# Kernel tuning notes

Measured on AMD Instinct MI355X. Metric: run time of the kernel, lower is better.

## Reference

```python
import jax, jax.numpy as jnp
import numpy as np

SIZES = [11793, 2948, 737, 184]   # vertices per mesh level, fine -> coarse
SPIRAL = [20, 14, 12, 9]          # spiral length per level
FILT = [128, 128, 64, 3]          # filters_dec[0]
LATENT = 128
BATCH = 16


def setup_inputs() -> dict:
    key = jax.random.key(0)
    ks = jax.random.split(key, 12)
    V = [s + 1 for s in SIZES]  # +1 dummy vertex per level
    inp = {}
    inp["z"] = jax.random.normal(ks[0], (BATCH, LATENT), jnp.float32)
    # dense upsampling matrices: level k+1 -> level k
    inp["U0"] = jax.random.normal(ks[1], (V[0], V[1]), jnp.float32) * 0.02
    inp["U1"] = jax.random.normal(ks[2], (V[1], V[2]), jnp.float32) * 0.02
    inp["U2"] = jax.random.normal(ks[3], (V[2], V[3]), jnp.float32) * 0.02
    # spiral index tables per level (shared across batch, values in [0, V))
    inp["S0"] = jax.random.randint(ks[4], (V[0], SPIRAL[0]), 0, V[0], dtype=jnp.int32)
    inp["S1"] = jax.random.randint(ks[5], (V[1], SPIRAL[1]), 0, V[1], dtype=jnp.int32)
    inp["S2"] = jax.random.randint(ks[6], (V[2], SPIRAL[2]), 0, V[2], dtype=jnp.int32)
    # fc_latent_dec: latent -> (sizes[-1]+1)*filters_dec[0][0]
    inp["Wfc"] = jax.random.normal(ks[7], (LATENT, V[3] * FILT[0]), jnp.float32) * 0.02
    inp["bfc"] = jnp.zeros((V[3] * FILT[0],), jnp.float32)
    # SpiralConv linear weights, stored (K*F_in, F_out), K-major flatten as in torch
    inp["W0"] = jax.random.normal(ks[8], (SPIRAL[2] * FILT[0], FILT[1]), jnp.float32) * 0.02
    inp["b0"] = jnp.zeros((FILT[1],), jnp.float32)
    inp["W1"] = jax.random.normal(ks[9], (SPIRAL[1] * FILT[1], FILT[2]), jnp.float32) * 0.02
    inp["b1"] = jnp.zeros((FILT[2],), jnp.float32)
    inp["W2"] = jax.random.normal(ks[10], (SPIRAL[0] * FILT[2], FILT[3]), jnp.float32) * 0.02
    inp["b2"] = jnp.zeros((FILT[3],), jnp.float32)
    return inp


def spiral_conv(x, S, W, b, elu):
    # x: (B, V, F); S: (V, K) vertex indices into the same level
    B, V, F = x.shape
    K = S.shape[1]
    g = jnp.take(x, S.reshape(-1), axis=1).reshape(B, V, K * F)  # gather, K-major flatten
    out = g @ W + b  # (B, V, F_out)
    if elu:
        out = jax.nn.elu(out)
    # zero out the dummy (last) vertex, as in Neural3DMM's zero_padding mask
    return out.at[:, -1, :].set(0.0)


def reference(z, U0, U1, U2, S0, S1, S2, Wfc, bfc, W0, b0, W1, b1, W2, b2):
    B = z.shape[0]
    x = (z @ Wfc + bfc).reshape(B, SIZES[-1] + 1, FILT[0])  # (B, 185, 128)
    x = jnp.einsum('vw,bwf->bvf', U2, x)                    # upsample -> (B, 738, 128)
    x = spiral_conv(x, S2, W0, b0, True)                    # (B, 738, 128)
    x = jnp.einsum('vw,bwf->bvf', U1, x)                    # (B, 2949, 128)
    x = spiral_conv(x, S1, W1, b1, True)                    # (B, 2949, 64)
    x = jnp.einsum('vw,bwf->bvf', U0, x)                    # (B, 11794, 64)
    x = spiral_conv(x, S0, W2, b2, False)                   # identity act -> (B, 11794, 3)
    return x
```

## Files before the change

kernel.cpp:

```cpp
#include <hip/hip_runtime.h>
#include <cmath>


#define NB 16

typedef __attribute__((ext_vector_type(8))) short bf16x8;
typedef __attribute__((ext_vector_type(4))) float f32x4;

__device__ __forceinline__ unsigned short f2bf(float x) {
    union { float f; unsigned u; } v; v.f = x;
    unsigned r = v.u + 0x7FFFu + ((v.u >> 16) & 1u);
    return (unsigned short)(r >> 16);
}
__device__ __forceinline__ void gload16(const void* src, void* dst) {
    __builtin_amdgcn_global_load_lds(
        (const __attribute__((address_space(1))) unsigned int*)src,
        (__attribute__((address_space(3))) unsigned int*)dst, 16, 0, 0);
}

__global__ __launch_bounds__(256) void cvt_u_all(
    const float* __restrict__ U0, const float* __restrict__ U1,
    const float* __restrict__ U2, unsigned short* __restrict__ Ub0,
    unsigned short* __restrict__ Ub1, unsigned short* __restrict__ Ub2) {
    int k = blockIdx.x * 256 + threadIdx.x;
    int r = blockIdx.y;
    const float* src;
    unsigned short* dst;
    int V, W, Wp, row;
    if (r < 11904) {
        src = U0; dst = Ub0; V = 11794; W = 2949; Wp = 2976; row = r;
    } else if (r < 11904 + 3072) {
        src = U1; dst = Ub1; V = 2949; W = 738; Wp = 768; row = r - 11904;
    } else {
        src = U2; dst = Ub2; V = 738; W = 185; Wp = 192; row = r - 11904 - 3072;
    }
    if (k >= Wp) return;
    float v = (row < V && k < W) ? src[(size_t)row * W + k] : 0.f;
    dst[(size_t)row * Wp + k] = f2bf(v);
}

__global__ __launch_bounds__(256) void cvt_misc(
    const float* __restrict__ W0, const float* __restrict__ W1,
    const float* __restrict__ W2, const int* __restrict__ S0,
    const int* __restrict__ S1, const int* __restrict__ S2,
    unsigned short* __restrict__ W0T, unsigned short* __restrict__ W1T,
    unsigned short* __restrict__ W2T, int* __restrict__ S0T,
    int* __restrict__ S1T, int* __restrict__ S2T) {
    const int N0 = 128 * 1536, N1 = 64 * 1792, N2 = 16 * 1288;
    const int N3 = 20 * 11794, N4 = 14 * 2949, N5 = 12 * 738;
    int id = blockIdx.x * 256 + threadIdx.x;
    if (id < N0) {
        int n = id / 1536, k = id - n * 1536;
        W0T[id] = f2bf(W0[(size_t)k * 128 + n]);
        return;
    }
    id -= N0;
    if (id < N1) {
        int n = id / 1792, k = id - n * 1792;
        W1T[id] = f2bf(W1[(size_t)k * 64 + n]);
        return;
    }
    id -= N1;
    if (id < N2) {
        int n = id / 1288, k = id - n * 1288;
        float v = (n < 3 && k < 1280) ? W2[(size_t)k * 3 + n] : 0.f;
        W2T[id] = f2bf(v);
        return;
    }
    id -= N2;
    if (id < N3) {
        int k = id / 11794, v = id - k * 11794;
        S0T[id] = S0[(size_t)v * 20 + k];
        return;
    }
    id -= N3;
    if (id < N4) {
        int k = id / 2949, v = id - k * 2949;
        S1T[id] = S1[(size_t)v * 14 + k];
        return;
    }
    id -= N4;
    if (id < N5) {
        int k = id / 738, v = id - k * 738;
        S2T[id] = S2[(size_t)v * 12 + k];
    }
}

__global__ __launch_bounds__(256) void fc_kernel(const float* __restrict__ z,
                                                 const float* __restrict__ Wfc,
                                                 const float* __restrict__ bfc,
                                                 unsigned short* __restrict__ x3T) {
    const int N = 185 * 128;
    __shared__ float zs[NB * 128];
    int t = threadIdx.x;
    for (int i = t; i < NB * 128; i += 256) zs[i] = z[i];
    __syncthreads();
    int n = blockIdx.x * 256 + t;
    if (n >= N) return;
    float acc[NB];
#pragma unroll
    for (int b = 0; b < NB; ++b) acc[b] = 0.f;
    for (int k = 0; k < 128; ++k) {
        float w = Wfc[k * N + n];
#pragma unroll
        for (int b = 0; b < NB; ++b) acc[b] = fmaf(zs[b * 128 + k], w, acc[b]);
    }
    float bv = bfc[n];
    int f = n & 127, v = n >> 7;
#pragma unroll
    for (int b = 0; b < NB; ++b)
        x3T[(size_t)(b * 128 + f) * 192 + v] = f2bf(acc[b] + bv);
    if (n < 7 * 128) {
        int vp = 185 + (n >> 7);
#pragma unroll
        for (int b = 0; b < NB; ++b)
            x3T[(size_t)(b * 128 + f) * 192 + vp] = 0;
    }
}

template<int FSH, int VP>
__global__ __launch_bounds__(256) void ups_mfma(
    const unsigned short* __restrict__ Ub, const unsigned short* __restrict__ xT,
    unsigned short* __restrict__ out,
    int WpA, int WpB, int nsteps, int gxsh, int q) {
    const int F = 1 << FSH;
    __shared__ __align__(16) unsigned short As[3][128 * 32];
    __shared__ __align__(16) unsigned short Bs[3][128 * 32];
    const int t = threadIdx.x;
    const int wv = t >> 6, lane = t & 63;
    const int lr = lane & 15;

    const int flat = blockIdx.x;
    const int wg = (flat & 7) * q + (flat >> 3);
    const int m0 = (wg >> gxsh) * 128;
    const int n0 = (wg & ((1 << gxsh) - 1)) * 128;

    const int srow = lane >> 2;
    const int schunk = (((lane & 3) - ((lane >> 3) & 3)) & 3) * 8;
    const int ii0 = wv * 2, ii1 = wv * 2 + 1;
    const unsigned short* asrc0 = Ub + (size_t)(m0 + ii0 * 16 + srow) * WpA + schunk;
    const unsigned short* asrc1 = Ub + (size_t)(m0 + ii1 * 16 + srow) * WpA + schunk;
    const unsigned short* bsrc0 = xT + (size_t)(n0 + ii0 * 16 + srow) * WpB + schunk;
    const unsigned short* bsrc1 = xT + (size_t)(n0 + ii1 * 16 + srow) * WpB + schunk;

    const int fslot = (((lane >> 4) + (lr >> 1)) & 3) * 8;
    const int wrow = (wv >> 1) * 64;
    const int wcol = (wv & 1) * 64;
    const int u0 = wv * 1024;

    f32x4 acc[4][4];
#pragma unroll
    for (int i = 0; i < 4; ++i)
#pragma unroll
        for (int j = 0; j < 4; ++j) acc[i][j] = {0.f, 0.f, 0.f, 0.f};

#define UPS_STAGE(off_, B_)                                             \
    {                                                                   \
        gload16(asrc0 + (off_), &As[B_][u0]);                           \
        gload16(bsrc0 + (off_), &Bs[B_][u0]);                           \
        gload16(asrc1 + (off_), &As[B_][u0 + 512]);                     \
        gload16(bsrc1 + (off_), &Bs[B_][u0 + 512]);                     \
    }
#define UPS_COMPUTE(B_)                                                 \
    {                                                                   \
        bf16x8 af[4], bg[4];                                            \
        _Pragma("unroll")                                               \
        for (int mt = 0; mt < 4; ++mt)                                  \
            af[mt] = *(const bf16x8*)&As[B_][(wrow + mt * 16 + lr) * 32 + fslot]; \
        _Pragma("unroll")                                               \
        for (int nt = 0; nt < 4; ++nt)                                  \
            bg[nt] = *(const bf16x8*)&Bs[B_][(wcol + nt * 16 + lr) * 32 + fslot]; \
        _Pragma("unroll")                                               \
        for (int mt = 0; mt < 4; ++mt)                                  \
            _Pragma("unroll")                                           \
            for (int nt = 0; nt < 4; ++nt)                              \
                acc[mt][nt] = __builtin_amdgcn_mfma_f32_16x16x32_bf16(  \
                    af[mt], bg[nt], acc[mt][nt], 0, 0, 0);              \
    }
#define UPS_WAIT4 asm volatile("s_waitcnt vmcnt(4)" ::: "memory"); __builtin_amdgcn_s_barrier();
#define UPS_WAIT0 asm volatile("s_waitcnt vmcnt(0)" ::: "memory"); __builtin_amdgcn_s_barrier();

    UPS_STAGE(0, 0);
    UPS_STAGE(32, 1);
    UPS_WAIT4;

    const int m = nsteps / 3;
    for (int it = 0; it < m - 1; ++it) {
        UPS_STAGE(64, 2);  UPS_COMPUTE(0); UPS_WAIT4;
        UPS_STAGE(96, 0);  UPS_COMPUTE(1); UPS_WAIT4;
        UPS_STAGE(128, 1); UPS_COMPUTE(2); UPS_WAIT4;
        asrc0 += 96; asrc1 += 96; bsrc0 += 96; bsrc1 += 96;
    }
    UPS_STAGE(64, 2);
    UPS_COMPUTE(0); UPS_WAIT4;
    UPS_COMPUTE(1); UPS_WAIT0;
    UPS_COMPUTE(2);
#undef UPS_STAGE
#undef UPS_COMPUTE
#undef UPS_WAIT4
#undef UPS_WAIT0

#pragma unroll
    for (int mt = 0; mt < 4; ++mt) {
        const int vb = m0 + wrow + mt * 16 + (lane >> 4) * 4;
#pragma unroll
        for (int nt = 0; nt < 4; ++nt) {
            const int col = n0 + wcol + nt * 16 + lr;
            const int b = col >> FSH, f = col & (F - 1);
            unsigned short* op = out + (size_t)b * VP * F + f;
#pragma unroll
            for (int j = 0; j < 4; ++j)
                op[(size_t)(vb + j) * F] = f2bf(acc[mt][nt][j]);
        }
    }
}

template<int VP, int NSTEPS, int KSP>
__global__ __launch_bounds__(64) void conv_mfma(
    const unsigned short* __restrict__ xu, const int* __restrict__ ST,
    const unsigned short* __restrict__ WT, const float* __restrict__ bias,
    unsigned short* __restrict__ outT,
    int VT, int Kdim, int Fout) {
    __shared__ __align__(16) unsigned short As[2][32 * 32];
    __shared__ __align__(16) unsigned short Bs[3][64 * 32];
    const int lane = threadIdx.x;
    const int lr = lane & 15;
    const int m0 = blockIdx.x * 32;
    const int n0 = blockIdx.y * 64;
    const int b = m0 / VP;
    const int v0 = m0 - b * VP;
    const unsigned short* xb = xu + (((size_t)b * VP) << 7);

    const int arow = lane >> 1;
    const int h = lane & 1;
    const int vg = (v0 + arow < VT) ? (v0 + arow) : (VT - 1);
    const int schunk = (((lane & 3) - ((lane >> 3) & 3)) & 3) * 8;
    const int fslot = (((lane >> 4) + (lr >> 1)) & 3) * 8;
    const int sw0 = arow * 32 + (((2 * h + 0 + ((lane >> 2) & 3)) & 3) * 8);
    const int sw1 = arow * 32 + (((2 * h + 1 + ((lane >> 2) & 3)) & 3) * 8);

    int idx[KSP];
#pragma unroll
    for (int k = 0; k < KSP; ++k) idx[k] = ST[(size_t)k * VT + vg];

    f32x4 acc[2][4];
#pragma unroll
    for (int i = 0; i < 2; ++i)
#pragma unroll
        for (int j = 0; j < 4; ++j) acc[i][j] = {0.f, 0.f, 0.f, 0.f};

    bf16x8 gA[2][2];

#define CC(AB_, BB_)                                                    \
    {                                                                   \
        bf16x8 af[2], bg[4];                                            \
        _Pragma("unroll")                                               \
        for (int mt = 0; mt < 2; ++mt)                                  \
            af[mt] = *(const bf16x8*)&As[AB_][(mt * 16 + lr) * 32 + fslot]; \
        _Pragma("unroll")                                               \
        for (int nt = 0; nt < 4; ++nt)                                  \
            bg[nt] = *(const bf16x8*)&Bs[BB_][(nt * 16 + lr) * 32 + fslot]; \
        _Pragma("unroll")                                               \
        for (int mt = 0; mt < 2; ++mt)                                  \
            _Pragma("unroll")                                           \
            for (int nt = 0; nt < 4; ++nt)                              \
                acc[mt][nt] = __builtin_amdgcn_mfma_f32_16x16x32_bf16(  \
                    af[mt], bg[nt], acc[mt][nt], 0, 0, 0);              \
    }

    {
        const unsigned short* p = xb + (((size_t)idx[0]) << 7) + h * 16;
        gA[0][0] = *(const bf16x8*)(p);
        gA[0][1] = *(const bf16x8*)(p + 8);
#pragma unroll
        for (int i = 0; i < 4; ++i) {
            const int n = n0 + i * 16 + (lane >> 2);
            gload16(WT + (size_t)n * Kdim + schunk, &Bs[0][i * 512]);
        }
#pragma unroll
        for (int i = 0; i < 4; ++i) {
            const int n = n0 + i * 16 + (lane >> 2);
            gload16(WT + (size_t)n * Kdim + 32 + schunk, &Bs[1][i * 512]);
        }
        *(bf16x8*)&As[0][sw0] = gA[0][0];
        *(bf16x8*)&As[0][sw1] = gA[0][1];
        asm volatile("s_waitcnt vmcnt(4)" ::: "memory");
    }

#pragma unroll
    for (int ts = 0; ts < NSTEPS - 2; ++ts) {
        const int tn1 = ts + 1, tn2 = ts + 2;
        {
            const unsigned short* p =
                xb + (((size_t)idx[tn1 >> 2]) << 7) + (tn1 & 3) * 32 + h * 16;
            gA[tn1 & 1][0] = *(const bf16x8*)(p);
            gA[tn1 & 1][1] = *(const bf16x8*)(p + 8);
        }
        {
            const int k0 = tn2 * 32;
#pragma unroll
            for (int i = 0; i < 4; ++i) {
                const int n = n0 + i * 16 + (lane >> 2);
                gload16(WT + (size_t)n * Kdim + k0 + schunk, &Bs[tn2 % 3][i * 512]);
            }
        }
        CC(ts & 1, ts % 3);
        asm volatile("s_waitcnt vmcnt(4)" ::: "memory");
        *(bf16x8*)&As[tn1 & 1][sw0] = gA[tn1 & 1][0];
        *(bf16x8*)&As[tn1 & 1][sw1] = gA[tn1 & 1][1];
    }
    {
        const int tn1 = NSTEPS - 1;
        const unsigned short* p =
            xb + (((size_t)idx[tn1 >> 2]) << 7) + (tn1 & 3) * 32 + h * 16;
        gA[tn1 & 1][0] = *(const bf16x8*)(p);
        gA[tn1 & 1][1] = *(const bf16x8*)(p + 8);
        CC((NSTEPS - 2) & 1, (NSTEPS - 2) % 3);
        asm volatile("s_waitcnt vmcnt(0)" ::: "memory");
        *(bf16x8*)&As[tn1 & 1][sw0] = gA[tn1 & 1][0];
        *(bf16x8*)&As[tn1 & 1][sw1] = gA[tn1 & 1][1];
    }
    CC((NSTEPS - 1) & 1, (NSTEPS - 1) % 3);
#undef CC

#pragma unroll
    for (int nt = 0; nt < 4; ++nt) {
        const int n = n0 + nt * 16 + lr;
        const float bv = bias[n];
        unsigned short* op = outT + (size_t)(b * Fout + n) * VP;
#pragma unroll
        for (int mt = 0; mt < 2; ++mt) {
            const int v = v0 + mt * 16 + (lane >> 4) * 4;
            ushort4 stv;
#pragma unroll
            for (int j = 0; j < 4; ++j) {
                float val = acc[mt][nt][j] + bv;
                val = val > 0.f ? val : expm1f(val);
                if (v + j == VT - 1) val = 0.f;
                ((unsigned short*)&stv)[j] = f2bf(val);
            }
            *(ushort4*)(op + v) = stv;
        }
    }
}

__global__ __launch_bounds__(64) void out_mfma(
    const unsigned short* __restrict__ xu, const int* __restrict__ ST,
    const unsigned short* __restrict__ W2T, const float* __restrict__ b2,
    float* __restrict__ out) {
    const int VT = 11794, VP = 11904, TPB = 372, NSTEPS = 40;
    __shared__ __align__(16) unsigned short As[2][32 * 32];
    const int lane = threadIdx.x;
    const int lr = lane & 15;
    const int lko = (lane >> 4) * 8;
    const int bm = blockIdx.x;
    const int b = bm / TPB;
    const int v0 = (bm - b * TPB) * 32;
    const unsigned short* xb = xu + ((size_t)b * VP << 6);

    const int arow = lane >> 1;
    const int h = lane & 1;
    const int v = v0 + arow;
    const int vg = v < VT ? v : VT - 1;
    const int sw0 = arow * 32 + (((2 * h + 0 + ((lane >> 2) & 3)) & 3) * 8);
    const int sw1 = arow * 32 + (((2 * h + 1 + ((lane >> 2) & 3)) & 3) * 8);
    const int fslot = (((lane >> 4) + (lr >> 1)) & 3) * 8;

    int idx[20];
#pragma unroll
    for (int k = 0; k < 20; ++k) idx[k] = ST[(size_t)k * VT + vg];

    f32x4 acc[2];
    acc[0] = {0.f, 0.f, 0.f, 0.f};
    acc[1] = {0.f, 0.f, 0.f, 0.f};

    const unsigned short* wrow = W2T + (size_t)lr * 1288 + lko;
    bf16x8 gA[2][2], bgr[2];

#define OC(AB_, WB_)                                                    \
    {                                                                   \
        bf16x8 af[2];                                                   \
        _Pragma("unroll")                                               \
        for (int mt = 0; mt < 2; ++mt)                                  \
            af[mt] = *(const bf16x8*)&As[AB_][(mt * 16 + lr) * 32 + fslot]; \
        _Pragma("unroll")                                               \
        for (int mt = 0; mt < 2; ++mt)                                  \
            acc[mt] = __builtin_amdgcn_mfma_f32_16x16x32_bf16(          \
                af[mt], bgr[WB_], acc[mt], 0, 0, 0);                    \
    }

    {
        const unsigned short* p = xb + (((size_t)idx[0]) << 6) + h * 16;
        gA[0][0] = *(const bf16x8*)(p);
        gA[0][1] = *(const bf16x8*)(p + 8);
        bgr[0] = *(const bf16x8*)(wrow);
        *(bf16x8*)&As[0][sw0] = gA[0][0];
        *(bf16x8*)&As[0][sw1] = gA[0][1];
    }

#pragma unroll
    for (int ts = 0; ts < NSTEPS - 1; ++ts) {
        const int tn = ts + 1;
        const unsigned short* p =
            xb + (((size_t)idx[tn >> 1]) << 6) + (tn & 1) * 32 + h * 16;
        gA[tn & 1][0] = *(const bf16x8*)(p);
        gA[tn & 1][1] = *(const bf16x8*)(p + 8);
        bgr[tn & 1] = *(const bf16x8*)(wrow + tn * 32);
        OC(ts & 1, ts & 1);
        *(bf16x8*)&As[tn & 1][sw0] = gA[tn & 1][0];
        *(bf16x8*)&As[tn & 1][sw1] = gA[tn & 1][1];
    }
    OC((NSTEPS - 1) & 1, (NSTEPS - 1) & 1);
#undef OC

    if (lr < 3) {
        const float bv = b2[lr];
#pragma unroll
        for (int mt = 0; mt < 2; ++mt) {
#pragma unroll
            for (int j = 0; j < 4; ++j) {
                const int vv = v0 + mt * 16 + (lane >> 4) * 4 + j;
                if (vv < VT) {
                    float val = acc[mt][j] + bv;
                    if (vv == VT - 1) val = 0.f;
                    out[((size_t)b * VT + vv) * 3 + lr] = val;
                }
            }
        }
    }
}

extern "C" void kernel_launch(void* const* d_in, const int* in_sizes, int n_in,
                              void* d_out, int out_size, void* d_ws, size_t ws_size,
                              hipStream_t stream) {
    const float* z   = (const float*)d_in[0];
    const float* U0  = (const float*)d_in[1];
    const float* U1  = (const float*)d_in[2];
    const float* U2  = (const float*)d_in[3];
    const int*   S0  = (const int*)d_in[4];
    const int*   S1  = (const int*)d_in[5];
    const int*   S2  = (const int*)d_in[6];
    const float* Wfc = (const float*)d_in[7];
    const float* bfc = (const float*)d_in[8];
    const float* W0  = (const float*)d_in[9];
    const float* b0  = (const float*)d_in[10];
    const float* W1  = (const float*)d_in[11];
    const float* b1  = (const float*)d_in[12];
    const float* W2  = (const float*)d_in[13];
    const float* b2  = (const float*)d_in[14];
    float* out = (float*)d_out;

    char* ws = (char*)d_ws;
    unsigned short* Ub0 = (unsigned short*)(ws + 0);
    unsigned short* Ub1 = (unsigned short*)(ws + 70852608);
    unsigned short* Ub2 = (unsigned short*)(ws + 75571200);
    unsigned short* x3T = (unsigned short*)(ws + 75866112);
    unsigned short* x2u = (unsigned short*)(ws + 76652544);
    unsigned short* x2T = (unsigned short*)(ws + 79798272);
    unsigned short* x1u = (unsigned short*)(ws + 82944000);
    unsigned short* x1T = (unsigned short*)(ws + 95526912);
    unsigned short* x0u = (unsigned short*)(ws + 101818368);
    unsigned short* W0T = (unsigned short*)(ws + 126197760);
    unsigned short* W1T = (unsigned short*)(ws + 126590976);
    int* S1T = (int*)(ws + 126820352);
    int* S2T = (int*)(ws + 126985504);
    int* S0T = (int*)(ws + 127020928);
    unsigned short* W2T = (unsigned short*)(ws + 127964448);

    cvt_u_all<<<dim3(12, 11904 + 3072 + 768), 256, 0, stream>>>(U0, U1, U2, Ub0, Ub1, Ub2);
    {
        const int total = 128 * 1536 + 64 * 1792 + 16 * 1288 +
                          20 * 11794 + 14 * 2949 + 12 * 738;
        cvt_misc<<<dim3((total + 255) / 256), 256, 0, stream>>>(
            W0, W1, W2, S0, S1, S2, W0T, W1T, W2T, S0T, S1T, S2T);
    }

    fc_kernel<<<dim3((185 * 128 + 255) / 256), 256, 0, stream>>>(z, Wfc, bfc, x3T);
    ups_mfma<7, 768><<<dim3(96), 256, 0, stream>>>(Ub2, x3T, x2u, 192, 192, 6, 4, 12);
    conv_mfma<768, 48, 12><<<dim3(384, 2), 64, 0, stream>>>(
        x2u, S2T, W0T, b0, x2T, 738, 1536, 128);
    ups_mfma<7, 3072><<<dim3(384), 256, 0, stream>>>(Ub1, x2T, x1u, 768, 768, 24, 4, 48);
    conv_mfma<3072, 56, 14><<<dim3(1536, 1), 64, 0, stream>>>(
        x1u, S1T, W1T, b1, x1T, 2949, 1792, 64);
    ups_mfma<6, 11904><<<dim3(744), 256, 0, stream>>>(Ub0, x1T, x0u, 2976, 3072, 93, 3, 93);
    out_mfma<<<dim3(16 * 372), 64, 0, stream>>>(x0u, S0T, W2T, b2, out);
}
```

Measured before the change: 353.6 us.

## Halve upsample GEMM N-tile and pack U conversion into grid-stride pairs

The upsampling MFMA kernel now uses 128x64 output tiles instead of 128x128, doubling the workgroup count for each level to improve occupancy and CU coverage. The cost is reloading A tiles twice as often. The fp32-to-bf16 conversion of the dense upsampling matrices now runs as a fixed 2048-block grid-stride kernel. Each thread converts two elements and writes one packed 32-bit word, replacing a huge 2D grid with one thread per element.

```diff
diff --git a/kernel.cpp b/kernel.cpp
--- a/kernel.cpp
+++ b/kernel.cpp
@@ -20,23 +20,43 @@
 
 __global__ __launch_bounds__(256) void cvt_u_all(
     const float* __restrict__ U0, const float* __restrict__ U1,
-    const float* __restrict__ U2, unsigned short* __restrict__ Ub0,
-    unsigned short* __restrict__ Ub1, unsigned short* __restrict__ Ub2) {
-    int k = blockIdx.x * 256 + threadIdx.x;
-    int r = blockIdx.y;
-    const float* src;
-    unsigned short* dst;
-    int V, W, Wp, row;
-    if (r < 11904) {
-        src = U0; dst = Ub0; V = 11794; W = 2949; Wp = 2976; row = r;
-    } else if (r < 11904 + 3072) {
-        src = U1; dst = Ub1; V = 2949; W = 738; Wp = 768; row = r - 11904;
-    } else {
-        src = U2; dst = Ub2; V = 738; W = 185; Wp = 192; row = r - 11904 - 3072;
-    }
-    if (k >= Wp) return;
-    float v = (row < V && k < W) ? src[(size_t)row * W + k] : 0.f;
-    dst[(size_t)row * Wp + k] = f2bf(v);
+    const float* __restrict__ U2, unsigned int* __restrict__ Ub0,
+    unsigned int* __restrict__ Ub1, unsigned int* __restrict__ Ub2) {
+    const unsigned nth = gridDim.x * 256u;
+    const unsigned tid = blockIdx.x * 256u + threadIdx.x;
+    for (unsigned p = tid; p < 11904u * 1488u; p += nth) {
+        unsigned row = p / 1488u;
+        unsigned k = (p - row * 1488u) * 2u;
+        float v0 = 0.f, v1 = 0.f;
+        if (row < 11794u) {
+            const float* s = U0 + (size_t)row * 2949u + k;
+            if (k < 2949u) v0 = s[0];
+            if (k + 1u < 2949u) v1 = s[1];
+        }
+        Ub0[p] = (unsigned)f2bf(v0) | ((unsigned)f2bf(v1) << 16);
+    }
+    for (unsigned p = tid; p < 3072u * 384u; p += nth) {
+        unsigned row = p / 384u;
+        unsigned k = (p - row * 384u) * 2u;
+        float v0 = 0.f, v1 = 0.f;
+        if (row < 2949u) {
+            const float* s = U1 + (size_t)row * 738u + k;
+            if (k < 738u) v0 = s[0];
+            if (k + 1u < 738u) v1 = s[1];
+        }
+        Ub1[p] = (unsigned)f2bf(v0) | ((unsigned)f2bf(v1) << 16);
+    }
+    for (unsigned p = tid; p < 768u * 96u; p += nth) {
+        unsigned row = p / 96u;
+        unsigned k = (p - row * 96u) * 2u;
+        float v0 = 0.f, v1 = 0.f;
+        if (row < 738u) {
+            const float* s = U2 + (size_t)row * 185u + k;
+            if (k < 185u) v0 = s[0];
+            if (k + 1u < 185u) v1 = s[1];
+        }
+        Ub2[p] = (unsigned)f2bf(v0) | ((unsigned)f2bf(v1) << 16);
+    }
 }
 
 __global__ __launch_bounds__(256) void cvt_misc(
@@ -125,7 +145,7 @@
     int WpA, int WpB, int nsteps, int gxsh, int q) {
     const int F = 1 << FSH;
     __shared__ __align__(16) unsigned short As[3][128 * 32];
-    __shared__ __align__(16) unsigned short Bs[3][128 * 32];
+    __shared__ __align__(16) unsigned short Bs[3][64 * 32];
     const int t = threadIdx.x;
     const int wv = t >> 6, lane = t & 63;
     const int lr = lane & 15;
@@ -133,78 +153,77 @@
     const int flat = blockIdx.x;
     const int wg = (flat & 7) * q + (flat >> 3);
     const int m0 = (wg >> gxsh) * 128;
-    const int n0 = (wg & ((1 << gxsh) - 1)) * 128;
+    const int n0 = (wg & ((1 << gxsh) - 1)) * 64;
 
     const int srow = lane >> 2;
     const int schunk = (((lane & 3) - ((lane >> 3) & 3)) & 3) * 8;
     const int ii0 = wv * 2, ii1 = wv * 2 + 1;
     const unsigned short* asrc0 = Ub + (size_t)(m0 + ii0 * 16 + srow) * WpA + schunk;
     const unsigned short* asrc1 = Ub + (size_t)(m0 + ii1 * 16 + srow) * WpA + schunk;
-    const unsigned short* bsrc0 = xT + (size_t)(n0 + ii0 * 16 + srow) * WpB + schunk;
-    const unsigned short* bsrc1 = xT + (size_t)(n0 + ii1 * 16 + srow) * WpB + schunk;
+    const unsigned short* bsrc0 = xT + (size_t)(n0 + wv * 16 + srow) * WpB + schunk;
 
     const int fslot = (((lane >> 4) + (lr >> 1)) & 3) * 8;
     const int wrow = (wv >> 1) * 64;
-    const int wcol = (wv & 1) * 64;
+    const int wcol = (wv & 1) * 32;
     const int u0 = wv * 1024;
-
-    f32x4 acc[4][4];
+    const int ub0 = wv * 512;
+
+    f32x4 acc[4][2];
 #pragma unroll
     for (int i = 0; i < 4; ++i)
 #pragma unroll
-        for (int j = 0; j < 4; ++j) acc[i][j] = {0.f, 0.f, 0.f, 0.f};
+        for (int j = 0; j < 2; ++j) acc[i][j] = {0.f, 0.f, 0.f, 0.f};
 
 #define UPS_STAGE(off_, B_)                                             \
     {                                                                   \
         gload16(asrc0 + (off_), &As[B_][u0]);                           \
-        gload16(bsrc0 + (off_), &Bs[B_][u0]);                           \
+        gload16(bsrc0 + (off_), &Bs[B_][ub0]);                          \
         gload16(asrc1 + (off_), &As[B_][u0 + 512]);                     \
-        gload16(bsrc1 + (off_), &Bs[B_][u0 + 512]);                     \
     }
 #define UPS_COMPUTE(B_)                                                 \
     {                                                                   \
-        bf16x8 af[4], bg[4];                                            \
+        bf16x8 af[4], bg[2];                                            \
         _Pragma("unroll")                                               \
         for (int mt = 0; mt < 4; ++mt)                                  \
             af[mt] = *(const bf16x8*)&As[B_][(wrow + mt * 16 + lr) * 32 + fslot]; \
         _Pragma("unroll")                                               \
-        for (int nt = 0; nt < 4; ++nt)                                  \
+        for (int nt = 0; nt < 2; ++nt)                                  \
             bg[nt] = *(const bf16x8*)&Bs[B_][(wcol + nt * 16 + lr) * 32 + fslot]; \
         _Pragma("unroll")                                               \
         for (int mt = 0; mt < 4; ++mt)                                  \
             _Pragma("unroll")                                           \
-            for (int nt = 0; nt < 4; ++nt)                              \
+            for (int nt = 0; nt < 2; ++nt)                              \
                 acc[mt][nt] = __builtin_amdgcn_mfma_f32_16x16x32_bf16(  \
                     af[mt], bg[nt], acc[mt][nt], 0, 0, 0);              \
     }
-#define UPS_WAIT4 asm volatile("s_waitcnt vmcnt(4)" ::: "memory"); __builtin_amdgcn_s_barrier();
+#define UPS_WAIT3 asm volatile("s_waitcnt vmcnt(3)" ::: "memory"); __builtin_amdgcn_s_barrier();
 #define UPS_WAIT0 asm volatile("s_waitcnt vmcnt(0)" ::: "memory"); __builtin_amdgcn_s_barrier();
 
     UPS_STAGE(0, 0);
     UPS_STAGE(32, 1);
-    UPS_WAIT4;
+    UPS_WAIT3;
 
     const int m = nsteps / 3;
     for (int it = 0; it < m - 1; ++it) {
-        UPS_STAGE(64, 2);  UPS_COMPUTE(0); UPS_WAIT4;
-        UPS_STAGE(96, 0);  UPS_COMPUTE(1); UPS_WAIT4;
-        UPS_STAGE(128, 1); UPS_COMPUTE(2); UPS_WAIT4;
-        asrc0 += 96; asrc1 += 96; bsrc0 += 96; bsrc1 += 96;
+        UPS_STAGE(64, 2);  UPS_COMPUTE(0); UPS_WAIT3;
+        UPS_STAGE(96, 0);  UPS_COMPUTE(1); UPS_WAIT3;
+        UPS_STAGE(128, 1); UPS_COMPUTE(2); UPS_WAIT3;
+        asrc0 += 96; asrc1 += 96; bsrc0 += 96;
     }
     UPS_STAGE(64, 2);
-    UPS_COMPUTE(0); UPS_WAIT4;
+    UPS_COMPUTE(0); UPS_WAIT3;
     UPS_COMPUTE(1); UPS_WAIT0;
     UPS_COMPUTE(2);
 #undef UPS_STAGE
 #undef UPS_COMPUTE
-#undef UPS_WAIT4
+#undef UPS_WAIT3
 #undef UPS_WAIT0
 
 #pragma unroll
     for (int mt = 0; mt < 4; ++mt) {
         const int vb = m0 + wrow + mt * 16 + (lane >> 4) * 4;
 #pragma unroll
-        for (int nt = 0; nt < 4; ++nt) {
+        for (int nt = 0; nt < 2; ++nt) {
             const int col = n0 + wcol + nt * 16 + lr;
             const int b = col >> FSH, f = col & (F - 1);
             unsigned short* op = out + (size_t)b * VP * F + f;
@@ -467,7 +486,8 @@
     int* S0T = (int*)(ws + 127020928);
     unsigned short* W2T = (unsigned short*)(ws + 127964448);
 
-    cvt_u_all<<<dim3(12, 11904 + 3072 + 768), 256, 0, stream>>>(U0, U1, U2, Ub0, Ub1, Ub2);
+    cvt_u_all<<<dim3(2048), 256, 0, stream>>>(U0, U1, U2,
+        (unsigned int*)Ub0, (unsigned int*)Ub1, (unsigned int*)Ub2);
     {
         const int total = 128 * 1536 + 64 * 1792 + 16 * 1288 +
                           20 * 11794 + 14 * 2949 + 12 * 738;
@@ -476,12 +496,12 @@
     }
 
     fc_kernel<<<dim3((185 * 128 + 255) / 256), 256, 0, stream>>>(z, Wfc, bfc, x3T);
-    ups_mfma<7, 768><<<dim3(96), 256, 0, stream>>>(Ub2, x3T, x2u, 192, 192, 6, 4, 12);
+    ups_mfma<7, 768><<<dim3(192), 256, 0, stream>>>(Ub2, x3T, x2u, 192, 192, 6, 5, 24);
     conv_mfma<768, 48, 12><<<dim3(384, 2), 64, 0, stream>>>(
         x2u, S2T, W0T, b0, x2T, 738, 1536, 128);
-    ups_mfma<7, 3072><<<dim3(384), 256, 0, stream>>>(Ub1, x2T, x1u, 768, 768, 24, 4, 48);
+    ups_mfma<7, 3072><<<dim3(768), 256, 0, stream>>>(Ub1, x2T, x1u, 768, 768, 24, 5, 96);
     conv_mfma<3072, 56, 14><<<dim3(1536, 1), 64, 0, stream>>>(
         x1u, S1T, W1T, b1, x1T, 2949, 1792, 64);
-    ups_mfma<6, 11904><<<dim3(744), 256, 0, stream>>>(Ub0, x1T, x0u, 2976, 3072, 93, 3, 93);
+    ups_mfma<6, 11904><<<dim3(1488), 256, 0, stream>>>(Ub0, x1T, x0u, 2976, 3072, 93, 4, 186);
     out_mfma<<<dim3(16 * 372), 64, 0, stream>>>(x0u, S0T, W2T, b2, out);
 }
```

Result: faster. 342.7 us (-3.1%).
